# Performance work log

Hardware: AMD Instinct MI355X
Metric: run time of the kernel (lower is better)

Reference implementation:

```python
import jax, jax.numpy as jnp
import numpy as np


def _lstm_last(x, wih, whh, bih, bhh):
    """PyTorch-semantics LSTM over x [B, T, I]; returns last hidden state [B, H].
    Gate order in weights: i, f, g, o (PyTorch convention)."""
    B = x.shape[0]
    H = whh.shape[1]
    b = bih + bhh

    def step(carry, xt):
        h, c = carry
        g = xt @ wih.T + h @ whh.T + b  # [B, 4H]
        i, f, gg, o = jnp.split(g, 4, axis=-1)
        c = jax.nn.sigmoid(f) * c + jax.nn.sigmoid(i) * jnp.tanh(gg)
        h = jax.nn.sigmoid(o) * jnp.tanh(c)
        return (h, c), None

    h0 = jnp.zeros((B, H), x.dtype)
    (h, _), _ = jax.lax.scan(step, (h0, h0), jnp.swapaxes(x, 0, 1))
    return h


def setup_inputs() -> dict:
    key = jax.random.key(0)
    ks = jax.random.split(key, 16)
    B, N, T = 512, 32, 50
    s = 0.05
    return {
        "agent_traj": jax.random.normal(ks[0], (B, T, 2), jnp.float32),
        "neighbour_traj": jax.random.normal(ks[1], (B, N, T, 2), jnp.float32),
        "a_wih": jax.random.normal(ks[2], (256, 2), jnp.float32) * s,
        "a_whh": jax.random.normal(ks[3], (256, 64), jnp.float32) * s,
        "a_bih": jax.random.normal(ks[4], (256,), jnp.float32) * s,
        "a_bhh": jax.random.normal(ks[5], (256,), jnp.float32) * s,
        "n_wih": jax.random.normal(ks[6], (256, 2), jnp.float32) * s,
        "n_whh": jax.random.normal(ks[7], (256, 64), jnp.float32) * s,
        "n_bih": jax.random.normal(ks[8], (256,), jnp.float32) * s,
        "n_bhh": jax.random.normal(ks[9], (256,), jnp.float32) * s,
        "d_wih": jax.random.normal(ks[10], (512, 128), jnp.float32) * s,
        "d_whh": jax.random.normal(ks[11], (512, 128), jnp.float32) * s,
        "d_bih": jax.random.normal(ks[12], (512,), jnp.float32) * s,
        "d_bhh": jax.random.normal(ks[13], (512,), jnp.float32) * s,
        "e_w": jax.random.normal(ks[14], (2, 128), jnp.float32) * s,
        "e_b": jax.random.normal(ks[15], (2,), jnp.float32) * s,
    }


def reference(agent_traj, neighbour_traj, a_wih, a_whh, a_bih, a_bhh,
              n_wih, n_whh, n_bih, n_bhh, d_wih, d_whh, d_bih, d_bhh, e_w, e_b):
    B, N, T, _ = neighbour_traj.shape
    # agent encoder: last hidden state [B, 64]
    agent_emb = _lstm_last(agent_traj, a_wih, a_whh, a_bih, a_bhh)
    # neighbour encoder: batch all B*N ragged sequences as one LSTM call, then mean over neighbours
    nh = _lstm_last(neighbour_traj.reshape(B * N, T, 2), n_wih, n_whh, n_bih, n_bhh)
    neigh_emb = nh.reshape(B, N, 64).mean(axis=1)  # [B, 64]

    h0 = jnp.concatenate([agent_emb, neigh_emb], axis=1)  # [B, 128]
    c0 = jnp.zeros_like(h0)
    db = d_bih + d_bhh

    def dec_step(carry, _):
        h, c = carry
        # LSTMCell with input = h itself
        g = h @ d_wih.T + h @ d_whh.T + db  # [B, 512]
        i, f, gg, o = jnp.split(g, 4, axis=-1)
        c = jax.nn.sigmoid(f) * c + jax.nn.sigmoid(i) * jnp.tanh(gg)
        h = jax.nn.sigmoid(o) * jnp.tanh(c)
        pred = h @ e_w.T + e_b  # [B, 2]
        return (h, c), pred

    _, preds = jax.lax.scan(dec_step, (h0, c0), None, length=30)  # [30, B, 2]
    return jnp.swapaxes(preds, 0, 1)  # [B, 30, 2]
```

## Files before the change

### kernel.cpp

```cpp
#include <hip/hip_runtime.h>
#include <hip/hip_bf16.h>


typedef __attribute__((ext_vector_type(8))) short bf16x8;
typedef __attribute__((ext_vector_type(4))) float f32x4;
typedef unsigned int uint;
typedef unsigned short ushort_t;

#define LOG2E  1.4426950408889634f
#define LOG2E2 2.8853900817779268f

__device__ __forceinline__ float rcp_fast(float x) { return __builtin_amdgcn_rcpf(x); }
__device__ __forceinline__ float exp2_fast(float x) { return __builtin_amdgcn_exp2f(x); }
__device__ __forceinline__ float sigf(float x) { return rcp_fast(1.0f + __expf(-x)); }
__device__ __forceinline__ float tanh_fast(float x) {
    x = fminf(fmaxf(x, -15.0f), 15.0f);
    float e = __expf(2.0f * x);
    return (e - 1.0f) * rcp_fast(e + 1.0f);
}
__device__ __forceinline__ ushort_t bf_hi(float f) {
    union { float f; uint u; } v; v.f = f;
    return (ushort_t)(v.u >> 16);
}
__device__ __forceinline__ ushort_t bf_rtn(float f) {
    union { float f; uint u; } v; v.f = f;
    return (ushort_t)((v.u + 0x7FFFu + ((v.u >> 16) & 1u)) >> 16);
}
__device__ __forceinline__ float bf_f(ushort_t h) {
    union { float f; uint u; } v; v.u = ((uint)h) << 16;
    return v.f;
}

__device__ __forceinline__ float cell_update_p(float xi, float xf, float xg,
                                               float xo, float& c) {
    float pi = exp2_fast(-xi);
    float pf = exp2_fast(-xf);
    float po = exp2_fast(-xo);
    float pg = exp2_fast(fminf(xg, 120.0f));
    float A = 1.0f + pf;
    float B = 1.0f + pi;
    float C = 1.0f + pg;
    float BC = B * C;
    float R  = rcp_fast(A * BC);
    float num = __builtin_fmaf(c, BC, (C - 2.0f) * A);
    float cc = num * R;
    c = cc;
    float e2 = exp2_fast(fminf(cc * LOG2E2, 120.0f));
    return (e2 - 1.0f) * rcp_fast((1.0f + po) * (e2 + 1.0f));
}

#define HS 36

__global__ __launch_bounds__(256, 2) void enc17_kernel(
    const float* __restrict__ ax, const float* __restrict__ nx,
    const float* __restrict__ a_wih, const float* __restrict__ a_whh,
    const float* __restrict__ a_bih, const float* __restrict__ a_bhh,
    const float* __restrict__ n_wih, const float* __restrict__ n_whh,
    const float* __restrict__ n_bih, const float* __restrict__ n_bhh,
    float* __restrict__ nh_out, float* __restrict__ ah_out)
{
    const int tid = threadIdx.x, blk = blockIdx.x;
    const bool agent = (blk >= 512);
    const int seq0 = (agent ? (blk - 512) : blk) * 32;
    const float* __restrict__ x   = agent ? ax : nx;
    const float* __restrict__ wih = agent ? a_wih : n_wih;
    const float* __restrict__ whh = agent ? a_whh : n_whh;
    const float* __restrict__ bih = agent ? a_bih : n_bih;
    const float* __restrict__ bhh = agent ? a_bhh : n_bhh;
    float* __restrict__ hout = agent ? ah_out : nh_out;

    const int lane = tid & 63, wv = tid >> 6;
    const int col = lane & 15, quad = lane >> 4;

    __shared__ __attribute__((aligned(16))) uint hb[2][32][HS];
    __shared__ __attribute__((aligned(16))) ushort_t xb[50][32][8];

    bf16x8 Aw[4][2];
    #pragma unroll
    for (int g = 0; g < 4; ++g) {
        const float sc = (g == 2) ? LOG2E2 : LOG2E;
        #pragma unroll
        for (int kt = 0; kt < 2; ++kt) {
            const float* p = whh + (size_t)(g * 64 + 16 * wv + col) * 64 + kt * 32 + quad * 8;
            float4 v0 = *(const float4*)p;
            float4 v1 = *(const float4*)(p + 4);
            float vv[8] = { v0.x, v0.y, v0.z, v0.w, v1.x, v1.y, v1.z, v1.w };
            bf16x8 h8;
            #pragma unroll
            for (int j = 0; j < 8; ++j) h8[j] = (short)bf_rtn(vv[j] * sc);
            Aw[g][kt] = h8;
        }
    }

    bf16x8 Ax[4];
    #pragma unroll
    for (int g = 0; g < 4; ++g) {
        const float sc = (g == 2) ? LOG2E2 : LOG2E;
        bf16x8 a;
        #pragma unroll
        for (int j = 0; j < 8; ++j) a[j] = 0;
        if (quad == 0) {
            const int row = g * 64 + 16 * wv + col;
            float w0 = wih[2 * row] * sc, w1 = wih[2 * row + 1] * sc;
            float b  = (bih[row] + bhh[row]) * sc;
            ushort_t w0h = bf_hi(w0), w1h = bf_hi(w1);
            ushort_t bh  = bf_hi(b);
            a[0] = (short)w0h;
            a[1] = (short)w1h;
            a[2] = (short)bf_hi(w0 - bf_f(w0h));
            a[3] = (short)bf_hi(w1 - bf_f(w1h));
            a[4] = (short)w0h;
            a[5] = (short)w1h;
            a[6] = (short)bh;
            a[7] = (short)bf_hi(b - bf_f(bh));
        }
        Ax[g] = a;
    }

    for (int idx = tid; idx < 50 * 32; idx += 256) {
        const int t = idx >> 5, s = idx & 31;
        const float* xp = x + (size_t)(seq0 + s) * 100 + 2 * t;
        float x0 = xp[0], x1 = xp[1];
        ushort_t h0 = bf_hi(x0), h1 = bf_hi(x1);
        ushort_t* e = &xb[t][s][0];
        e[0] = h0; e[1] = h1;
        e[2] = h0; e[3] = h1;
        e[4] = bf_hi(x0 - bf_f(h0));
        e[5] = bf_hi(x1 - bf_f(h1));
        e[6] = 0x3F80; e[7] = 0x3F80;
    }
    for (int i = tid; i < 32 * HS; i += 256) (&hb[0][0][0])[i] = 0u;
    __syncthreads();

    float c0[4] = {0.f, 0.f, 0.f, 0.f};
    float c1[4] = {0.f, 0.f, 0.f, 0.f};
    float hv0[4], hv1[4];
    bf16x8 Bx0 = *(const bf16x8*)&xb[0][col][0];
    bf16x8 Bx1 = *(const bf16x8*)&xb[0][col + 16][0];

    for (int t = 0; t < 50; ++t) {
        const int cur = t & 1, nxt = cur ^ 1;

        const f32x4 z4 = {0.f, 0.f, 0.f, 0.f};
        f32x4 accA[4], accB[4];
        #pragma unroll
        for (int g = 0; g < 4; ++g) {
            accA[g] = __builtin_amdgcn_mfma_f32_16x16x32_bf16(Ax[g], Bx0, z4, 0, 0, 0);
            accB[g] = __builtin_amdgcn_mfma_f32_16x16x32_bf16(Ax[g], Bx1, z4, 0, 0, 0);
        }

        #pragma unroll
        for (int kt = 0; kt < 2; ++kt) {
            bf16x8 Bh0 = *(const bf16x8*)&hb[cur][col][kt * 16 + quad * 4];
            bf16x8 Bh1 = *(const bf16x8*)&hb[cur][col + 16][kt * 16 + quad * 4];
            #pragma unroll
            for (int g = 0; g < 4; ++g) {
                accA[g] = __builtin_amdgcn_mfma_f32_16x16x32_bf16(Aw[g][kt], Bh0, accA[g], 0, 0, 0);
                accB[g] = __builtin_amdgcn_mfma_f32_16x16x32_bf16(Aw[g][kt], Bh1, accB[g], 0, 0, 0);
            }
        }

        #pragma unroll
        for (int r = 0; r < 4; ++r)
            hv0[r] = cell_update_p(accA[0][r], accA[1][r], accA[2][r], accA[3][r], c0[r]);
        #pragma unroll
        for (int r = 0; r < 4; ++r)
            hv1[r] = cell_update_p(accB[0][r], accB[1][r], accB[2][r], accB[3][r], c1[r]);

        {
            union { __hip_bfloat162 b; uint u; } q0, q1;
            uint2 hi2;
            const int di = 8 * wv + 2 * quad;
            q0.b = __float22bfloat162_rn(make_float2(hv0[0], hv0[1]));
            q1.b = __float22bfloat162_rn(make_float2(hv0[2], hv0[3]));
            hi2.x = q0.u; hi2.y = q1.u;
            *(uint2*)&hb[nxt][col][di] = hi2;
            q0.b = __float22bfloat162_rn(make_float2(hv1[0], hv1[1]));
            q1.b = __float22bfloat162_rn(make_float2(hv1[2], hv1[3]));
            hi2.x = q0.u; hi2.y = q1.u;
            *(uint2*)&hb[nxt][col + 16][di] = hi2;
        }
        if (t < 49) {
            Bx0 = *(const bf16x8*)&xb[t + 1][col][0];
            Bx1 = *(const bf16x8*)&xb[t + 1][col + 16][0];
        }
        __syncthreads();
    }

    {
        float4 o4 = make_float4(hv0[0], hv0[1], hv0[2], hv0[3]);
        *(float4*)(hout + (size_t)(seq0 + col) * 64 + 16 * wv + 4 * quad) = o4;
        o4 = make_float4(hv1[0], hv1[1], hv1[2], hv1[3]);
        *(float4*)(hout + (size_t)(seq0 + 16 + col) * 64 + 16 * wv + 4 * quad) = o4;
    }
}

__global__ __launch_bounds__(512) void dec17_kernel(
    const float* __restrict__ ah, const float* __restrict__ nh,
    const float* __restrict__ d_wih, const float* __restrict__ d_whh,
    const float* __restrict__ d_bih, const float* __restrict__ d_bhh,
    const float* __restrict__ e_w, const float* __restrict__ e_b,
    float* __restrict__ out)
{
    const int tid = threadIdx.x;
    const int blk = blockIdx.x;

    const int u  = tid >> 2;
    const int tt = tid & 3;
    const int r  = tt * 128 + u;

    float w[128];
    #pragma unroll
    for (int k = 0; k < 128; k += 4) {
        float4 aa = *(const float4*)(d_wih + r * 128 + k);
        float4 bb = *(const float4*)(d_whh + r * 128 + k);
        w[k]   = aa.x + bb.x;
        w[k+1] = aa.y + bb.y;
        w[k+2] = aa.z + bb.z;
        w[k+3] = aa.w + bb.w;
    }
    const float bias = d_bih[r] + d_bhh[r];

    __shared__ float hs[2][128];
    __shared__ float cs[2][128];
    __shared__ float gs[2][512];
    __shared__ float ews[2][128];
    __shared__ float ebs[2];

    if (tid < 256) {
        const int s = tid >> 7, j = tid & 127;
        const int gseq = blk * 2 + s;
        float v;
        if (j < 64) {
            v = ah[(size_t)gseq * 64 + j];
        } else {
            float acc = 0.0f;
            for (int n = 0; n < 32; ++n)
                acc += nh[(size_t)(gseq * 32 + n) * 64 + (j - 64)];
            v = acc * (1.0f / 32.0f);
        }
        hs[s][j] = v;
        cs[s][j] = 0.0f;
        ews[s][j] = e_w[tid];
    }
    if (tid < 2) ebs[tid] = e_b[tid];
    __syncthreads();

    for (int t = 0; t < 30; ++t) {
        #pragma unroll
        for (int s = 0; s < 2; ++s) {
            const float4* hp = (const float4*)(&hs[s][0]);
            float a0 = 0.f, a1 = 0.f, a2 = 0.f, a3 = 0.f;
            #pragma unroll
            for (int k = 0; k < 32; ++k) {
                float4 h4 = hp[k];
                a0 = __builtin_fmaf(w[4*k+0], h4.x, a0);
                a1 = __builtin_fmaf(w[4*k+1], h4.y, a1);
                a2 = __builtin_fmaf(w[4*k+2], h4.z, a2);
                a3 = __builtin_fmaf(w[4*k+3], h4.w, a3);
            }
            gs[s][tid] = bias + ((a0 + a1) + (a2 + a3));
        }
        __syncthreads();
        if (tid < 256) {
            const int s = tid >> 7, j = tid & 127;
            float4 g4 = *(const float4*)(&gs[s][4 * j]);
            float ig = sigf(g4.x), fg = sigf(g4.y);
            float gg = tanh_fast(g4.z), og = sigf(g4.w);
            float cc = fg * cs[s][j] + ig * gg;
            cs[s][j] = cc;
            hs[s][j] = og * tanh_fast(cc);
        }
        __syncthreads();
        {
            const int wv = tid >> 6, l = tid & 63;
            if (wv < 4) {
                const int s = wv >> 1, o = wv & 1;
                float p = hs[s][l] * ews[o][l] + hs[s][64 + l] * ews[o][64 + l];
                #pragma unroll
                for (int off = 32; off > 0; off >>= 1) p += __shfl_down(p, off);
                if (l == 0) out[((size_t)(blk * 2 + s) * 30 + t) * 2 + o] = p + ebs[o];
            }
        }
    }
}

extern "C" void kernel_launch(void* const* d_in, const int* in_sizes, int n_in,
                              void* d_out, int out_size, void* d_ws, size_t ws_size,
                              hipStream_t stream)
{
    const float* agent_traj = (const float*)d_in[0];
    const float* neigh_traj = (const float*)d_in[1];
    const float* a_wih = (const float*)d_in[2];
    const float* a_whh = (const float*)d_in[3];
    const float* a_bih = (const float*)d_in[4];
    const float* a_bhh = (const float*)d_in[5];
    const float* n_wih = (const float*)d_in[6];
    const float* n_whh = (const float*)d_in[7];
    const float* n_bih = (const float*)d_in[8];
    const float* n_bhh = (const float*)d_in[9];
    const float* d_wih = (const float*)d_in[10];
    const float* d_whh = (const float*)d_in[11];
    const float* d_bih = (const float*)d_in[12];
    const float* d_bhh = (const float*)d_in[13];
    const float* e_w   = (const float*)d_in[14];
    const float* e_b   = (const float*)d_in[15];
    float* out = (float*)d_out;

    float* nh_ws = (float*)d_ws;
    float* ah_ws = nh_ws + 16384 * 64;

    enc17_kernel<<<dim3(512 + 16), dim3(256), 0, stream>>>(
        agent_traj, neigh_traj,
        a_wih, a_whh, a_bih, a_bhh,
        n_wih, n_whh, n_bih, n_bhh,
        nh_ws, ah_ws);

    dec17_kernel<<<dim3(256), dim3(512), 0, stream>>>(
        ah_ws, nh_ws, d_wih, d_whh, d_bih, d_bhh, e_w, e_b, out);
}
```

Baseline: 258.4 us.

## Software-pipeline two sequence halves in LSTM encoder to overlap MFMA with cell math

Each encoder block's 32 sequences are split into two 16-sequence halves, each with its own hidden-state buffer. The halves are staggered by half a step, so the MFMA gate matmuls of one half are issued while the transcendental cell update of the other runs. This is meant to hide the serial dependency latency between matrix and vector work in the recurrence. In exchange there are two barriers per timestep instead of one and extra prologue code.

```diff
diff --git a/kernel.cpp b/kernel.cpp
--- a/kernel.cpp
+++ b/kernel.cpp
@@ -51,7 +51,7 @@
 
 #define HS 36
 
-__global__ __launch_bounds__(256, 2) void enc17_kernel(
+__global__ __launch_bounds__(256, 2) void enc18_kernel(
     const float* __restrict__ ax, const float* __restrict__ nx,
     const float* __restrict__ a_wih, const float* __restrict__ a_whh,
     const float* __restrict__ a_bih, const float* __restrict__ a_bhh,
@@ -72,7 +72,8 @@
     const int lane = tid & 63, wv = tid >> 6;
     const int col = lane & 15, quad = lane >> 4;
 
-    __shared__ __attribute__((aligned(16))) uint hb[2][32][HS];
+    __shared__ __attribute__((aligned(16))) uint hbA[2][16][HS];
+    __shared__ __attribute__((aligned(16))) uint hbB[2][16][HS];
     __shared__ __attribute__((aligned(16))) ushort_t xb[50][32][8];
 
     bf16x8 Aw[4][2];
@@ -92,7 +93,7 @@
         }
     }
 
-    bf16x8 Ax[4];
+    bf16x8 Axf[4];
     #pragma unroll
     for (int g = 0; g < 4; ++g) {
         const float sc = (g == 2) ? LOG2E2 : LOG2E;
@@ -114,7 +115,7 @@
             a[6] = (short)bh;
             a[7] = (short)bf_hi(b - bf_f(bh));
         }
-        Ax[g] = a;
+        Axf[g] = a;
     }
 
     for (int idx = tid; idx < 50 * 32; idx += 256) {
@@ -129,73 +130,94 @@
         e[5] = bf_hi(x1 - bf_f(h1));
         e[6] = 0x3F80; e[7] = 0x3F80;
     }
-    for (int i = tid; i < 32 * HS; i += 256) (&hb[0][0][0])[i] = 0u;
+    for (int i = tid; i < 16 * HS; i += 256) {
+        (&hbA[0][0][0])[i] = 0u;
+        (&hbB[0][0][0])[i] = 0u;
+    }
     __syncthreads();
 
-    float c0[4] = {0.f, 0.f, 0.f, 0.f};
-    float c1[4] = {0.f, 0.f, 0.f, 0.f};
-    float hv0[4], hv1[4];
-    bf16x8 Bx0 = *(const bf16x8*)&xb[0][col][0];
-    bf16x8 Bx1 = *(const bf16x8*)&xb[0][col + 16][0];
+    float cA[4] = {0.f, 0.f, 0.f, 0.f};
+    float cB[4] = {0.f, 0.f, 0.f, 0.f};
+    float hvA[4], hvB[4];
+    bf16x8 BxA = *(const bf16x8*)&xb[0][col][0];
+    bf16x8 BxB = *(const bf16x8*)&xb[0][col + 16][0];
+
+    const f32x4 z4 = {0.f, 0.f, 0.f, 0.f};
+    f32x4 accA[4], accB[4];
+
+    #pragma unroll
+    for (int g = 0; g < 4; ++g)
+        accA[g] = __builtin_amdgcn_mfma_f32_16x16x32_bf16(Axf[g], BxA, z4, 0, 0, 0);
+    #pragma unroll
+    for (int kt = 0; kt < 2; ++kt) {
+        bf16x8 Bh = *(const bf16x8*)&hbA[0][col][kt * 16 + quad * 4];
+        #pragma unroll
+        for (int g = 0; g < 4; ++g)
+            accA[g] = __builtin_amdgcn_mfma_f32_16x16x32_bf16(Aw[g][kt], Bh, accA[g], 0, 0, 0);
+    }
+    BxA = *(const bf16x8*)&xb[1][col][0];
 
     for (int t = 0; t < 50; ++t) {
         const int cur = t & 1, nxt = cur ^ 1;
 
-        const f32x4 z4 = {0.f, 0.f, 0.f, 0.f};
-        f32x4 accA[4], accB[4];
-        #pragma unroll
-        for (int g = 0; g < 4; ++g) {
-            accA[g] = __builtin_amdgcn_mfma_f32_16x16x32_bf16(Ax[g], Bx0, z4, 0, 0, 0);
-            accB[g] = __builtin_amdgcn_mfma_f32_16x16x32_bf16(Ax[g], Bx1, z4, 0, 0, 0);
-        }
-
+        #pragma unroll
+        for (int g = 0; g < 4; ++g)
+            accB[g] = __builtin_amdgcn_mfma_f32_16x16x32_bf16(Axf[g], BxB, z4, 0, 0, 0);
         #pragma unroll
         for (int kt = 0; kt < 2; ++kt) {
-            bf16x8 Bh0 = *(const bf16x8*)&hb[cur][col][kt * 16 + quad * 4];
-            bf16x8 Bh1 = *(const bf16x8*)&hb[cur][col + 16][kt * 16 + quad * 4];
-            #pragma unroll
-            for (int g = 0; g < 4; ++g) {
-                accA[g] = __builtin_amdgcn_mfma_f32_16x16x32_bf16(Aw[g][kt], Bh0, accA[g], 0, 0, 0);
-                accB[g] = __builtin_amdgcn_mfma_f32_16x16x32_bf16(Aw[g][kt], Bh1, accB[g], 0, 0, 0);
-            }
-        }
-
+            bf16x8 Bh = *(const bf16x8*)&hbB[cur][col][kt * 16 + quad * 4];
+            #pragma unroll
+            for (int g = 0; g < 4; ++g)
+                accB[g] = __builtin_amdgcn_mfma_f32_16x16x32_bf16(Aw[g][kt], Bh, accB[g], 0, 0, 0);
+        }
         #pragma unroll
         for (int r = 0; r < 4; ++r)
-            hv0[r] = cell_update_p(accA[0][r], accA[1][r], accA[2][r], accA[3][r], c0[r]);
-        #pragma unroll
-        for (int r = 0; r < 4; ++r)
-            hv1[r] = cell_update_p(accB[0][r], accB[1][r], accB[2][r], accB[3][r], c1[r]);
-
+            hvA[r] = cell_update_p(accA[0][r], accA[1][r], accA[2][r], accA[3][r], cA[r]);
         {
             union { __hip_bfloat162 b; uint u; } q0, q1;
-            uint2 hi2;
-            const int di = 8 * wv + 2 * quad;
-            q0.b = __float22bfloat162_rn(make_float2(hv0[0], hv0[1]));
-            q1.b = __float22bfloat162_rn(make_float2(hv0[2], hv0[3]));
-            hi2.x = q0.u; hi2.y = q1.u;
-            *(uint2*)&hb[nxt][col][di] = hi2;
-            q0.b = __float22bfloat162_rn(make_float2(hv1[0], hv1[1]));
-            q1.b = __float22bfloat162_rn(make_float2(hv1[2], hv1[3]));
-            hi2.x = q0.u; hi2.y = q1.u;
-            *(uint2*)&hb[nxt][col + 16][di] = hi2;
-        }
+            q0.b = __float22bfloat162_rn(make_float2(hvA[0], hvA[1]));
+            q1.b = __float22bfloat162_rn(make_float2(hvA[2], hvA[3]));
+            uint2 hi2; hi2.x = q0.u; hi2.y = q1.u;
+            *(uint2*)&hbA[nxt][col][8 * wv + 2 * quad] = hi2;
+        }
+        if (t < 49) BxB = *(const bf16x8*)&xb[t + 1][col + 16][0];
+        __syncthreads();
+
         if (t < 49) {
-            Bx0 = *(const bf16x8*)&xb[t + 1][col][0];
-            Bx1 = *(const bf16x8*)&xb[t + 1][col + 16][0];
+            #pragma unroll
+            for (int g = 0; g < 4; ++g)
+                accA[g] = __builtin_amdgcn_mfma_f32_16x16x32_bf16(Axf[g], BxA, z4, 0, 0, 0);
+            #pragma unroll
+            for (int kt = 0; kt < 2; ++kt) {
+                bf16x8 Bh = *(const bf16x8*)&hbA[nxt][col][kt * 16 + quad * 4];
+                #pragma unroll
+                for (int g = 0; g < 4; ++g)
+                    accA[g] = __builtin_amdgcn_mfma_f32_16x16x32_bf16(Aw[g][kt], Bh, accA[g], 0, 0, 0);
+            }
+            if (t < 48) BxA = *(const bf16x8*)&xb[t + 2][col][0];
+        }
+        #pragma unroll
+        for (int r = 0; r < 4; ++r)
+            hvB[r] = cell_update_p(accB[0][r], accB[1][r], accB[2][r], accB[3][r], cB[r]);
+        {
+            union { __hip_bfloat162 b; uint u; } q0, q1;
+            q0.b = __float22bfloat162_rn(make_float2(hvB[0], hvB[1]));
+            q1.b = __float22bfloat162_rn(make_float2(hvB[2], hvB[3]));
+            uint2 hi2; hi2.x = q0.u; hi2.y = q1.u;
+            *(uint2*)&hbB[nxt][col][8 * wv + 2 * quad] = hi2;
         }
         __syncthreads();
     }
 
     {
-        float4 o4 = make_float4(hv0[0], hv0[1], hv0[2], hv0[3]);
+        float4 o4 = make_float4(hvA[0], hvA[1], hvA[2], hvA[3]);
         *(float4*)(hout + (size_t)(seq0 + col) * 64 + 16 * wv + 4 * quad) = o4;
-        o4 = make_float4(hv1[0], hv1[1], hv1[2], hv1[3]);
+        o4 = make_float4(hvB[0], hvB[1], hvB[2], hvB[3]);
         *(float4*)(hout + (size_t)(seq0 + 16 + col) * 64 + 16 * wv + 4 * quad) = o4;
     }
 }
 
-__global__ __launch_bounds__(512) void dec17_kernel(
+__global__ __launch_bounds__(512) void dec18_kernel(
     const float* __restrict__ ah, const float* __restrict__ nh,
     const float* __restrict__ d_wih, const float* __restrict__ d_whh,
     const float* __restrict__ d_bih, const float* __restrict__ d_bhh,
@@ -310,12 +332,12 @@
     float* nh_ws = (float*)d_ws;
     float* ah_ws = nh_ws + 16384 * 64;
 
-    enc17_kernel<<<dim3(512 + 16), dim3(256), 0, stream>>>(
+    enc18_kernel<<<dim3(512 + 16), dim3(256), 0, stream>>>(
         agent_traj, neigh_traj,
         a_wih, a_whh, a_bih, a_bhh,
         n_wih, n_whh, n_bih, n_bhh,
         nh_ws, ah_ws);
 
-    dec17_kernel<<<dim3(256), dim3(512), 0, stream>>>(
+    dec18_kernel<<<dim3(256), dim3(512), 0, stream>>>(
         ah_ws, nh_ws, d_wih, d_whh, d_bih, d_bhh, e_w, e_b, out);
 }
```

New measurement: 264.6 us. +2.4%, slower.
